# Optimization experiments

Hardware: AMD Instinct MI355X
Metric: run time of the kernel (lower is better)

The kernel has to match this reference:

```python
import jax, jax.numpy as jnp
import numpy as np

NUM_FEATURES = 602
NUM_CLASSES = 41
HIDDEN = 8
HEADS1 = 8
HEADS2 = 1
N_NODES = 100000
N_EDGES = 1600000
NEG_SLOPE = 0.2  # PyG GATConv default leaky_relu slope
EPS = 1e-16      # PyG softmax denominator epsilon


def gat_conv(x, edge_index, W, att_src, att_dst, bias, heads, out_ch, concat):
    """Faithful PyG GATConv forward (eval mode, dropout disabled).
    x: [N, F_in], edge_index: [2, E] with row0=src, row1=dst.
    W: [F_in, heads*out_ch], att_src/att_dst: [heads, out_ch], bias: [heads*out_ch] or [out_ch].
    """
    N = x.shape[0]
    h = (x @ W).reshape(N, heads, out_ch)              # [N, H, C]
    a_src = jnp.einsum('nhc,hc->nh', h, att_src)       # [N, H]
    a_dst = jnp.einsum('nhc,hc->nh', h, att_dst)       # [N, H]
    src, dst = edge_index[0], edge_index[1]
    e = jax.nn.leaky_relu(a_src[src] + a_dst[dst], NEG_SLOPE)  # [E, H]
    # segment softmax over incoming edges of each dst node
    m = jax.ops.segment_max(e, dst, num_segments=N)    # [N, H]
    e = jnp.exp(e - m[dst])
    denom = jax.ops.segment_sum(e, dst, num_segments=N)  # [N, H]
    alpha = e / (denom[dst] + EPS)                     # [E, H]
    msg = h[src] * alpha[:, :, None]                   # [E, H, C]
    out = jax.ops.segment_sum(msg, dst, num_segments=N)  # [N, H, C]
    if concat:
        out = out.reshape(N, heads * out_ch)
    else:
        out = out.mean(axis=1)
    return out + bias


def setup_inputs() -> dict:
    key = jax.random.key(0)
    ks = jax.random.split(key, 10)
    x = jax.random.normal(ks[0], (N_NODES, NUM_FEATURES), dtype=jnp.float32)
    edge_index = jax.random.randint(ks[1], (2, N_EDGES), 0, N_NODES, dtype=jnp.int64)
    s = 0.1
    W1 = jax.random.normal(ks[2], (NUM_FEATURES, HEADS1 * HIDDEN), dtype=jnp.float32) * s
    att_src1 = jax.random.normal(ks[3], (HEADS1, HIDDEN), dtype=jnp.float32) * s
    att_dst1 = jax.random.normal(ks[4], (HEADS1, HIDDEN), dtype=jnp.float32) * s
    b1 = jnp.zeros((HEADS1 * HIDDEN,), dtype=jnp.float32)
    W2 = jax.random.normal(ks[5], (HEADS1 * HIDDEN, HEADS2 * NUM_CLASSES), dtype=jnp.float32) * s
    att_src2 = jax.random.normal(ks[6], (HEADS2, NUM_CLASSES), dtype=jnp.float32) * s
    att_dst2 = jax.random.normal(ks[7], (HEADS2, NUM_CLASSES), dtype=jnp.float32) * s
    b2 = jnp.zeros((NUM_CLASSES,), dtype=jnp.float32)
    return {"x": x, "edge_index": edge_index, "W1": W1, "att_src1": att_src1,
            "att_dst1": att_dst1, "b1": b1, "W2": W2, "att_src2": att_src2,
            "att_dst2": att_dst2, "b2": b2}


def reference(x, edge_index, W1, att_src1, att_dst1, b1, W2, att_src2, att_dst2, b2):
    # eval mode: all F.dropout calls are identity
    h = gat_conv(x, edge_index, W1, att_src1, att_dst1, b1, HEADS1, HIDDEN, concat=True)
    h = jax.nn.elu(h)
    h = gat_conv(h, edge_index, W2, att_src2, att_dst2, b2, HEADS2, NUM_CLASSES, concat=False)
    return jax.nn.log_softmax(h, axis=1)
```

## Files before the change

### kernel.cpp

```cpp
#include <hip/hip_runtime.h>
#include <math.h>

#define NN 100000
#define NE 1600000
#define F_IN 602
#define H1 8
#define C1 8
#define F_MID 64
#define NC 41
#define H2_LD 48
#define NEG_SLOPE 0.2f
#define WT_LD 640
#define GB1 ((NN + 63) / 64)
#define DGB 1024
#define ATB ((NN * H1 + 255) / 256)

#define LRELU(x) fmaxf((x), NEG_SLOPE * (x))

typedef __attribute__((ext_vector_type(8))) short short8;
typedef __attribute__((ext_vector_type(4))) float f32x4;

__device__ inline unsigned short f2bf(float f) {
    unsigned u = __builtin_bit_cast(unsigned, f);
    unsigned r = (u + 0x7FFFu + ((u >> 16) & 1u)) >> 16;
    return (unsigned short)r;
}
__device__ inline float bf2f(unsigned short u) {
    unsigned v = ((unsigned)u) << 16;
    return __builtin_bit_cast(float, v);
}

__global__ void zero_kernel(int4* __restrict__ p, int n4)
{
    int i = blockIdx.x * blockDim.x + threadIdx.x;
    if (i < n4) p[i] = make_int4(0, 0, 0, 0);
}

__global__ void prep_wt_kernel(const float* __restrict__ W, unsigned short* __restrict__ Wt)
{
    int idx = blockIdx.x * blockDim.x + threadIdx.x;
    if (idx >= F_MID * WT_LD) return;
    int col = idx / WT_LD, k = idx % WT_LD;
    Wt[idx] = (k < F_IN) ? f2bf(W[k * F_MID + col]) : (unsigned short)0;
}

__global__ __launch_bounds__(256) void mega1_kernel(
    const float* __restrict__ x, const unsigned short* __restrict__ Wt,
    unsigned short* __restrict__ h1b,
    const int* __restrict__ dst, int* __restrict__ deg, int* __restrict__ rank,
    int N, int E)
{
    __shared__ unsigned short As[64][40];
    __shared__ unsigned short Bs[64][40];

    int bid = blockIdx.x;
    int t = threadIdx.x;

    if (bid < DGB) {
        for (int e = bid * 256 + t; e < E; e += DGB * 256)
            rank[e] = atomicAdd(&deg[dst[e]], 1);
        return;
    }

    int lane = t & 63;
    int w = t >> 6;
    int l16 = lane & 15, lg = lane >> 4;
    int n0 = (bid - DGB) * 64;

    int arow = t >> 2, aseg = t & 3;
    int grow = n0 + arow;
    const float* xrow = x + (size_t)(grow < N ? grow : 0) * F_IN + aseg * 8;
    int bcol = t >> 2;
    const unsigned short* wrow = Wt + (size_t)bcol * WT_LD + aseg * 8;

    f32x4 acc[4] = {};
    float2 av[4];
    uint4  bv;

    #pragma unroll
    for (int i = 0; i < 4; ++i) av[i] = *(const float2*)(xrow + i * 2);
    bv = *(const uint4*)(wrow);

    for (int kt = 0; kt < 19; ++kt) {
        __syncthreads();
        {
            unsigned short tmp[8];
            #pragma unroll
            for (int i = 0; i < 4; ++i) {
                tmp[i * 2]     = f2bf(av[i].x);
                tmp[i * 2 + 1] = f2bf(av[i].y);
            }
            *(uint4*)(&As[arow][aseg * 8]) = *(uint4*)tmp;
            *(uint4*)(&Bs[bcol][aseg * 8]) = bv;
        }
        __syncthreads();

        if (kt < 18) {
            int k0 = (kt + 1) * 32;
            if (kt + 1 < 18) {
                #pragma unroll
                for (int i = 0; i < 4; ++i) av[i] = *(const float2*)(xrow + k0 + i * 2);
            } else {
                #pragma unroll
                for (int i = 0; i < 4; ++i) {
                    int k = k0 + aseg * 8 + i * 2;
                    float a = (k < F_IN)     ? xrow[k0 + i * 2]     : 0.f;
                    float b = (k + 1 < F_IN) ? xrow[k0 + i * 2 + 1] : 0.f;
                    av[i] = make_float2(a, b);
                }
            }
            bv = *(const uint4*)(wrow + k0);
        }

        short8 afrag = *(const short8*)(&As[w * 16 + l16][lg * 8]);
        short8 bfrag[4];
        #pragma unroll
        for (int n = 0; n < 4; ++n)
            bfrag[n] = *(const short8*)(&Bs[n * 16 + l16][lg * 8]);
        #pragma unroll
        for (int n = 0; n < 4; ++n)
            acc[n] = __builtin_amdgcn_mfma_f32_16x16x32_bf16(afrag, bfrag[n], acc[n], 0, 0, 0);
    }

    #pragma unroll
    for (int r = 0; r < 4; ++r) {
        int row = n0 + w * 16 + lg * 4 + r;
        if (row < N) {
            #pragma unroll
            for (int n = 0; n < 4; ++n)
                h1b[(size_t)row * F_MID + n * 16 + l16] = f2bf(acc[n][r]);
        }
    }
}

__global__ void scan1_kernel(const int* __restrict__ deg, int* __restrict__ bsum, int N)
{
    int b = blockIdx.x, t = threadIdx.x;
    int base = b * 1024 + t * 16;
    int s = 0;
    #pragma unroll
    for (int i = 0; i < 16; ++i) { int idx = base + i; if (idx < N) s += deg[idx]; }
    #pragma unroll
    for (int o = 32; o > 0; o >>= 1) s += __shfl_down(s, o);
    if (t == 0) bsum[b] = s;
}

__global__ void scan2_kernel(const int* __restrict__ bsum, int* __restrict__ boff,
                             int nb, int* __restrict__ offs, int N, int E)
{
    __shared__ int buf[128];
    int t = threadIdx.x;
    int v = (t < nb) ? bsum[t] : 0;
    buf[t] = v;
    __syncthreads();
    for (int o = 1; o < 128; o <<= 1) {
        int u = (t >= o) ? buf[t - o] : 0;
        __syncthreads();
        buf[t] += u;
        __syncthreads();
    }
    if (t < nb) boff[t] = buf[t] - v;
    if (t == 0) offs[N] = E;
}

__global__ void scan3_kernel(const int* __restrict__ deg, const int* __restrict__ boff,
                             int* __restrict__ offs, int N)
{
    int b = blockIdx.x, t = threadIdx.x;
    int base = b * 1024 + t * 16;
    int loc[16];
    int s = 0;
    #pragma unroll
    for (int i = 0; i < 16; ++i) {
        int idx = base + i;
        loc[i] = (idx < N) ? deg[idx] : 0;
        s += loc[i];
    }
    int inc = s;
    #pragma unroll
    for (int o = 1; o < 64; o <<= 1) {
        int u = __shfl_up(inc, o);
        if (t >= o) inc += u;
    }
    int run = inc - s + boff[b];
    #pragma unroll
    for (int i = 0; i < 16; ++i) {
        int idx = base + i;
        if (idx < N) offs[idx] = run;
        run += loc[i];
    }
}

__global__ void mega2_kernel(
    const unsigned short* __restrict__ h1b,
    const float* __restrict__ attD,
    float* __restrict__ adst,
    const int* __restrict__ src, const int* __restrict__ dst,
    const int* __restrict__ rank, const int* __restrict__ offs,
    int* __restrict__ srcs, int N, int E)
{
    int bid = blockIdx.x, t = threadIdx.x;
    if (bid < DGB) {
        for (int e = bid * 256 + t; e < E; e += DGB * 256)
            srcs[offs[dst[e]] + rank[e]] = src[e];
        return;
    }
    int idx = (bid - DGB) * 256 + t;
    if (idx >= N * H1) return;
    int n = idx >> 3, hh = idx & 7;
    float d = 0.f;
    #pragma unroll
    for (int c = 0; c < C1; ++c)
        d += bf2f(h1b[n * F_MID + hh * C1 + c]) * attD[hh * C1 + c];
    adst[idx] = d;
}

__global__ void agg1_kernel(const int* __restrict__ offs, const int* __restrict__ srcs,
                            const unsigned short* __restrict__ h1b,
                            const float* __restrict__ attS,
                            const float* __restrict__ adst,
                            const float* __restrict__ b1,
                            float* __restrict__ out1, int N)
{
    int wave = (blockIdx.x * blockDim.x + threadIdx.x) >> 6;
    int lane = threadIdx.x & 63;
    if (wave >= N) return;
    int n = wave;
    int hh = lane >> 3;
    int beg = offs[n], end = offs[n + 1];
    float ad = adst[n * H1 + hh];
    float attv = attS[lane];

    float m = -INFINITY, den = 0.f, acc = 0.f;
    int i = beg;
    for (; i + 8 <= end; i += 8) {
        int s[8];
        #pragma unroll
        for (int j = 0; j < 8; ++j) s[j] = srcs[i + j];
        float v[8];
        #pragma unroll
        for (int j = 0; j < 8; ++j) v[j] = bf2f(h1b[(size_t)s[j] * F_MID + lane]);
        float e[8];
        #pragma unroll
        for (int j = 0; j < 8; ++j) {
            float tt = v[j] * attv;
            tt += __shfl_xor(tt, 1);
            tt += __shfl_xor(tt, 2);
            tt += __shfl_xor(tt, 4);
            e[j] = LRELU(tt + ad);
        }
        float m8 = fmaxf(fmaxf(fmaxf(e[0], e[1]), fmaxf(e[2], e[3])),
                         fmaxf(fmaxf(e[4], e[5]), fmaxf(e[6], e[7])));
        float mn = fmaxf(m, m8);
        float sc = __expf(m - mn);
        float p[8];
        #pragma unroll
        for (int j = 0; j < 8; ++j) p[j] = __expf(e[j] - mn);
        den = den * sc + (((p[0] + p[1]) + (p[2] + p[3])) + ((p[4] + p[5]) + (p[6] + p[7])));
        acc = acc * sc + (((p[0] * v[0] + p[1] * v[1]) + (p[2] * v[2] + p[3] * v[3]))
                        + ((p[4] * v[4] + p[5] * v[5]) + (p[6] * v[6] + p[7] * v[7])));
        m = mn;
    }
    for (; i < end; ++i) {
        int s = srcs[i];
        float hv = bf2f(h1b[(size_t)s * F_MID + lane]);
        float tt = hv * attv;
        tt += __shfl_xor(tt, 1);
        tt += __shfl_xor(tt, 2);
        tt += __shfl_xor(tt, 4);
        float e = LRELU(tt + ad);
        float mn = fmaxf(m, e);
        float sc = __expf(m - mn);
        float p  = __expf(e - mn);
        den = den * sc + p;
        acc = acc * sc + p * hv;
        m = mn;
    }
    float inv = 1.f / (den + 1e-16f);
    float v = acc * inv + b1[lane];
    out1[n * F_MID + lane] = v > 0.f ? v : expm1f(v);
}

__global__ __launch_bounds__(256) void gemm2_kernel(
    const float* __restrict__ out1, const float* __restrict__ W2,
    float* __restrict__ h2p, int N)
{
    __shared__ float ws[F_MID * NC];
    for (int i = threadIdx.x; i < F_MID * NC; i += 256) ws[i] = W2[i];
    __syncthreads();
    int idx = blockIdx.x * blockDim.x + threadIdx.x;
    if (idx >= N * NC) return;
    int n = idx / NC, j = idx % NC;
    const float* row = out1 + n * F_MID;
    float acc = 0.f;
    #pragma unroll
    for (int k = 0; k < F_MID; ++k) acc += row[k] * ws[k * NC + j];
    h2p[(size_t)n * H2_LD + j] = acc;
}

__global__ void attn2_kernel(float* __restrict__ h2p,
                             const float* __restrict__ attS,
                             const float* __restrict__ attD,
                             float* __restrict__ adst, int N)
{
    int n = blockIdx.x * blockDim.x + threadIdx.x;
    if (n >= N) return;
    float s = 0.f, d = 0.f;
    #pragma unroll
    for (int j = 0; j < NC; ++j) {
        float v = h2p[(size_t)n * H2_LD + j];
        s += v * attS[j];
        d += v * attD[j];
    }
    h2p[(size_t)n * H2_LD + NC] = s;
    adst[n] = d;
}

__global__ void agg2_kernel(const int* __restrict__ offs, const int* __restrict__ srcs,
                            const float* __restrict__ h2p,
                            const float* __restrict__ adst,
                            const float* __restrict__ b2,
                            float* __restrict__ out, int N)
{
    int wave = (blockIdx.x * blockDim.x + threadIdx.x) >> 6;
    int lane = threadIdx.x & 63;
    if (wave >= N) return;
    int n = wave;
    int beg = offs[n], end = offs[n + 1];
    float ad = adst[n];
    bool act = lane < NC;
    int li = act ? lane : NC;

    float m = -INFINITY, den = 0.f, acc = 0.f;
    int i = beg;
    for (; i + 8 <= end; i += 8) {
        int s[8];
        #pragma unroll
        for (int j = 0; j < 8; ++j) s[j] = srcs[i + j];
        float hv[8];
        #pragma unroll
        for (int j = 0; j < 8; ++j) hv[j] = h2p[(size_t)s[j] * H2_LD + li];
        float a[8];
        #pragma unroll
        for (int j = 0; j < 8; ++j) a[j] = __shfl(hv[j], NC);
        float e[8];
        #pragma unroll
        for (int j = 0; j < 8; ++j) e[j] = LRELU(a[j] + ad);
        float m8 = fmaxf(fmaxf(fmaxf(e[0], e[1]), fmaxf(e[2], e[3])),
                         fmaxf(fmaxf(e[4], e[5]), fmaxf(e[6], e[7])));
        float mn = fmaxf(m, m8);
        float sc = __expf(m - mn);
        float p[8];
        #pragma unroll
        for (int j = 0; j < 8; ++j) p[j] = __expf(e[j] - mn);
        den = den * sc + (((p[0] + p[1]) + (p[2] + p[3])) + ((p[4] + p[5]) + (p[6] + p[7])));
        acc = acc * sc + (((p[0] * hv[0] + p[1] * hv[1]) + (p[2] * hv[2] + p[3] * hv[3]))
                        + ((p[4] * hv[4] + p[5] * hv[5]) + (p[6] * hv[6] + p[7] * hv[7])));
        m = mn;
    }
    for (; i < end; ++i) {
        int s = srcs[i];
        float hv = h2p[(size_t)s * H2_LD + li];
        float a = __shfl(hv, NC);
        float e = LRELU(a + ad);
        float mn = fmaxf(m, e);
        float sc = __expf(m - mn);
        float p  = __expf(e - mn);
        den = den * sc + p;
        acc = acc * sc + p * hv;
        m = mn;
    }
    float inv = 1.f / (den + 1e-16f);
    float v = act ? acc * inv + b2[lane] : -INFINITY;
    float mm = v;
    #pragma unroll
    for (int o = 32; o > 0; o >>= 1) mm = fmaxf(mm, __shfl_xor(mm, o));
    float ex = act ? __expf(v - mm) : 0.f;
    float S = ex;
    #pragma unroll
    for (int o = 32; o > 0; o >>= 1) S += __shfl_xor(S, o);
    if (act) out[n * NC + lane] = v - mm - logf(S);
}

extern "C" void kernel_launch(void* const* d_in, const int* in_sizes, int n_in,
                              void* d_out, int out_size, void* d_ws, size_t ws_size,
                              hipStream_t stream)
{
    const float* x     = (const float*)d_in[0];
    const int*   ei    = (const int*)  d_in[1];
    const float* W1    = (const float*)d_in[2];
    const float* attS1 = (const float*)d_in[3];
    const float* attD1 = (const float*)d_in[4];
    const float* b1    = (const float*)d_in[5];
    const float* W2    = (const float*)d_in[6];
    const float* attS2 = (const float*)d_in[7];
    const float* attD2 = (const float*)d_in[8];
    const float* b2    = (const float*)d_in[9];
    float* out = (float*)d_out;

    const int N = NN, E = NE;
    const int* src = ei;
    const int* dst = ei + E;

    char* p = (char*)d_ws;
    auto alloc = [&](size_t bytes) { char* r = p; p += (bytes + 255) & ~255ull; return r; };
    unsigned short* h1b = (unsigned short*)alloc((size_t)N * F_MID * 2);
    float* adst1 = (float*)alloc((size_t)N * H1 * 4);
    float* out1  = (float*)alloc((size_t)N * F_MID * 4);
    float* h2p   = (float*)alloc((size_t)N * H2_LD * 4);
    float* adst2 = (float*)alloc((size_t)N * 4);
    int*   deg   = (int*)alloc((size_t)N * 4);
    int*   rank  = (int*)alloc((size_t)E * 4);
    int*   offs  = (int*)alloc((size_t)(N + 1) * 4);
    int*   srcs  = (int*)alloc((size_t)E * 4);
    unsigned short* Wt = (unsigned short*)alloc((size_t)F_MID * WT_LD * 2);
    const int NB = (N + 1023) / 1024;
    int*   bsum  = (int*)alloc((size_t)NB * 4);
    int*   boff  = (int*)alloc((size_t)NB * 4);

    zero_kernel<<<(N / 4 + 255) / 256, 256, 0, stream>>>((int4*)deg, N / 4);
    prep_wt_kernel<<<(F_MID * WT_LD + 255) / 256, 256, 0, stream>>>(W1, Wt);
    mega1_kernel<<<DGB + GB1, 256, 0, stream>>>(x, Wt, h1b, dst, deg, rank, N, E);
    scan1_kernel<<<NB, 64, 0, stream>>>(deg, bsum, N);
    scan2_kernel<<<1, 128, 0, stream>>>(bsum, boff, NB, offs, N, E);
    scan3_kernel<<<NB, 64, 0, stream>>>(deg, boff, offs, N);
    mega2_kernel<<<DGB + ATB, 256, 0, stream>>>(
        h1b, attD1, adst1, src, dst, rank, offs, srcs, N, E);
    agg1_kernel<<<(N * 64 + 255) / 256, 256, 0, stream>>>(
        offs, srcs, h1b, attS1, adst1, b1, out1, N);
    gemm2_kernel<<<(N * NC + 255) / 256, 256, 0, stream>>>(out1, W2, h2p, N);
    attn2_kernel<<<(N + 255) / 256, 256, 0, stream>>>(h2p, attS2, attD2, adst2, N);
    agg2_kernel<<<(N * 64 + 255) / 256, 256, 0, stream>>>(offs, srcs, h2p, adst2, b2, out, N);
}
```

Before: 412.0 us.

## Pipeline GEMM loads via async global_load_lds with triple-buffered LDS slab

The first-layer x@W GEMM now uses `global_load_lds` to copy x (fp32) and Wt (bf16) tiles straight into a three-stage LDS ring. It waits with explicit vmcnt and barriers instead of staging through registers with a double `__syncthreads` per step. The fp32-to-bf16 conversion moves to after the LDS read. The final partial K tile is loaded directly from global memory. This is meant to hide global memory latency and cut register staging, but each x load instruction now touches 64 different rows with 4-byte elements, which may hurt coalescing.

```diff
diff --git a/kernel.cpp b/kernel.cpp
--- a/kernel.cpp
+++ b/kernel.cpp
@@ -16,6 +16,8 @@
 #define ATB ((NN * H1 + 255) / 256)
 
 #define LRELU(x) fmaxf((x), NEG_SLOPE * (x))
+#define GLOBAL_AS __attribute__((address_space(1)))
+#define LDS_AS    __attribute__((address_space(3)))
 
 typedef __attribute__((ext_vector_type(8))) short short8;
 typedef __attribute__((ext_vector_type(4))) float f32x4;
@@ -50,8 +52,7 @@
     const int* __restrict__ dst, int* __restrict__ deg, int* __restrict__ rank,
     int N, int E)
 {
-    __shared__ unsigned short As[64][40];
-    __shared__ unsigned short Bs[64][40];
+    __shared__ __align__(16) unsigned char slab[3 * 12288];
 
     int bid = blockIdx.x;
     int t = threadIdx.x;
@@ -67,56 +68,71 @@
     int l16 = lane & 15, lg = lane >> 4;
     int n0 = (bid - DGB) * 64;
 
-    int arow = t >> 2, aseg = t & 3;
-    int grow = n0 + arow;
-    const float* xrow = x + (size_t)(grow < N ? grow : 0) * F_IN + aseg * 8;
-    int bcol = t >> 2;
-    const unsigned short* wrow = Wt + (size_t)bcol * WT_LD + aseg * 8;
+    int arow = n0 + lane;  if (arow >= N) arow = N - 1;
+    const float* xl = x + (size_t)arow * F_IN;
+    const unsigned short* wl = Wt + (size_t)lane * WT_LD;
+
+    auto issue = [&](int k0, int s) {
+        unsigned char* sb = slab + s * 12288;
+        #pragma unroll
+        for (int i = 0; i < 8; ++i)
+            __builtin_amdgcn_global_load_lds(
+                (const GLOBAL_AS void*)(xl + k0 + w * 8 + i),
+                (LDS_AS void*)(sb + (w * 8 + i) * 256), 4, 0, 0);
+        __builtin_amdgcn_global_load_lds(
+            (const GLOBAL_AS void*)(wl + k0 + w * 8),
+            (LDS_AS void*)(sb + 8192 + w * 1024), 16, 0, 0);
+    };
 
     f32x4 acc[4] = {};
-    float2 av[4];
-    uint4  bv;
-
-    #pragma unroll
-    for (int i = 0; i < 4; ++i) av[i] = *(const float2*)(xrow + i * 2);
-    bv = *(const uint4*)(wrow);
-
-    for (int kt = 0; kt < 19; ++kt) {
-        __syncthreads();
-        {
-            unsigned short tmp[8];
-            #pragma unroll
-            for (int i = 0; i < 4; ++i) {
-                tmp[i * 2]     = f2bf(av[i].x);
-                tmp[i * 2 + 1] = f2bf(av[i].y);
-            }
-            *(uint4*)(&As[arow][aseg * 8]) = *(uint4*)tmp;
-            *(uint4*)(&Bs[bcol][aseg * 8]) = bv;
+
+    issue(0, 0); issue(32, 1); issue(64, 2);
+    asm volatile("s_waitcnt vmcnt(18)" ::: "memory");
+    __builtin_amdgcn_s_barrier();
+
+    for (int kt = 0; kt <= 17; ++kt) {
+        int s = kt % 3;
+        const unsigned char* sb = slab + s * 12288;
+
+        float af[8];
+        #pragma unroll
+        for (int j = 0; j < 8; ++j)
+            af[j] = *(const float*)(sb + (((lg * 8 + j) * 64) + (w * 16 + l16)) * 4);
+        short8 afrag;
+        #pragma unroll
+        for (int j = 0; j < 8; ++j) afrag[j] = (short)f2bf(af[j]);
+        short8 bfrag[4];
+        #pragma unroll
+        for (int n = 0; n < 4; ++n)
+            bfrag[n] = *(const short8*)(sb + 8192 + (lg * 64 + n * 16 + l16) * 16);
+        #pragma unroll
+        for (int n = 0; n < 4; ++n)
+            acc[n] = __builtin_amdgcn_mfma_f32_16x16x32_bf16(afrag, bfrag[n], acc[n], 0, 0, 0);
+
+        __builtin_amdgcn_s_barrier();
+
+        if (kt + 3 <= 17) issue((kt + 3) * 32, s);
+
+        if (kt <= 14)      asm volatile("s_waitcnt vmcnt(18)" ::: "memory");
+        else if (kt == 15) asm volatile("s_waitcnt vmcnt(9)"  ::: "memory");
+        else               asm volatile("s_waitcnt vmcnt(0)"  ::: "memory");
+        __builtin_amdgcn_s_barrier();
+    }
+
+    {
+        const int k0 = 576;
+        int r = n0 + w * 16 + l16;  if (r >= N) r = N - 1;
+        const float* xr = x + (size_t)r * F_IN;
+        short8 afrag;
+        #pragma unroll
+        for (int i = 0; i < 8; ++i) {
+            int k = k0 + lg * 8 + i;
+            afrag[i] = (short)f2bf(k < F_IN ? xr[k] : 0.f);
         }
-        __syncthreads();
-
-        if (kt < 18) {
-            int k0 = (kt + 1) * 32;
-            if (kt + 1 < 18) {
-                #pragma unroll
-                for (int i = 0; i < 4; ++i) av[i] = *(const float2*)(xrow + k0 + i * 2);
-            } else {
-                #pragma unroll
-                for (int i = 0; i < 4; ++i) {
-                    int k = k0 + aseg * 8 + i * 2;
-                    float a = (k < F_IN)     ? xrow[k0 + i * 2]     : 0.f;
-                    float b = (k + 1 < F_IN) ? xrow[k0 + i * 2 + 1] : 0.f;
-                    av[i] = make_float2(a, b);
-                }
-            }
-            bv = *(const uint4*)(wrow + k0);
-        }
-
-        short8 afrag = *(const short8*)(&As[w * 16 + l16][lg * 8]);
         short8 bfrag[4];
         #pragma unroll
         for (int n = 0; n < 4; ++n)
-            bfrag[n] = *(const short8*)(&Bs[n * 16 + l16][lg * 8]);
+            bfrag[n] = *(const short8*)(Wt + (size_t)(n * 16 + l16) * WT_LD + k0 + lg * 8);
         #pragma unroll
         for (int n = 0; n < 4; ++n)
             acc[n] = __builtin_amdgcn_mfma_f32_16x16x32_bf16(afrag, bfrag[n], acc[n], 0, 0, 0);
```

Measured after the change: 484.9 us. 1.18x slower.

## Double GEMM K-tile to 64 and merge zeroing into weight-prep kernel

Applied to the files above, without the earlier changes.

The first-layer GEMM now stages 64 K-elements per iteration instead of 32, so it needs 10 loop iterations instead of 19 and half as many barrier pairs. Each iteration issues two MFMA k-steps, and each thread loads twice as much data per stage. The degree-zeroing kernel is folded into the weight transpose kernel, removing one launch. The larger tiles add register and LDS use, which may lower occupancy.

```diff
diff --git a/kernel.cpp b/kernel.cpp
--- a/kernel.cpp
+++ b/kernel.cpp
@@ -30,18 +30,17 @@
     return __builtin_bit_cast(float, v);
 }
 
-__global__ void zero_kernel(int4* __restrict__ p, int n4)
-{
-    int i = blockIdx.x * blockDim.x + threadIdx.x;
-    if (i < n4) p[i] = make_int4(0, 0, 0, 0);
-}
-
-__global__ void prep_wt_kernel(const float* __restrict__ W, unsigned short* __restrict__ Wt)
+__global__ void prep_kernel(const float* __restrict__ W, unsigned short* __restrict__ Wt,
+                            int4* __restrict__ degv, int ndeg4)
 {
     int idx = blockIdx.x * blockDim.x + threadIdx.x;
-    if (idx >= F_MID * WT_LD) return;
-    int col = idx / WT_LD, k = idx % WT_LD;
-    Wt[idx] = (k < F_IN) ? f2bf(W[k * F_MID + col]) : (unsigned short)0;
+    if (idx < F_MID * WT_LD) {
+        int col = idx / WT_LD, k = idx % WT_LD;
+        Wt[idx] = (k < F_IN) ? f2bf(W[k * F_MID + col]) : (unsigned short)0;
+    } else {
+        int z = idx - F_MID * WT_LD;
+        if (z < ndeg4) degv[z] = make_int4(0, 0, 0, 0);
+    }
 }
 
 __global__ __launch_bounds__(256) void mega1_kernel(
@@ -50,8 +49,8 @@
     const int* __restrict__ dst, int* __restrict__ deg, int* __restrict__ rank,
     int N, int E)
 {
-    __shared__ unsigned short As[64][40];
-    __shared__ unsigned short Bs[64][40];
+    __shared__ unsigned short As[64][72];
+    __shared__ unsigned short Bs[64][72];
 
     int bid = blockIdx.x;
     int t = threadIdx.x;
@@ -69,57 +68,64 @@
 
     int arow = t >> 2, aseg = t & 3;
     int grow = n0 + arow;
-    const float* xrow = x + (size_t)(grow < N ? grow : 0) * F_IN + aseg * 8;
+    const float* xrow = x + (size_t)(grow < N ? grow : 0) * F_IN + aseg * 16;
     int bcol = t >> 2;
-    const unsigned short* wrow = Wt + (size_t)bcol * WT_LD + aseg * 8;
+    const unsigned short* wrow = Wt + (size_t)bcol * WT_LD + aseg * 16;
 
     f32x4 acc[4] = {};
-    float2 av[4];
-    uint4  bv;
-
-    #pragma unroll
-    for (int i = 0; i < 4; ++i) av[i] = *(const float2*)(xrow + i * 2);
-    bv = *(const uint4*)(wrow);
-
-    for (int kt = 0; kt < 19; ++kt) {
+    float2 av[8];
+    uint4  bv[2];
+
+    #pragma unroll
+    for (int i = 0; i < 8; ++i) av[i] = *(const float2*)(xrow + i * 2);
+    bv[0] = *(const uint4*)(wrow);
+    bv[1] = *(const uint4*)(wrow + 8);
+
+    for (int kt = 0; kt < 10; ++kt) {
         __syncthreads();
         {
-            unsigned short tmp[8];
+            unsigned short tmp[16];
             #pragma unroll
-            for (int i = 0; i < 4; ++i) {
+            for (int i = 0; i < 8; ++i) {
                 tmp[i * 2]     = f2bf(av[i].x);
                 tmp[i * 2 + 1] = f2bf(av[i].y);
             }
-            *(uint4*)(&As[arow][aseg * 8]) = *(uint4*)tmp;
-            *(uint4*)(&Bs[bcol][aseg * 8]) = bv;
+            *(uint4*)(&As[arow][aseg * 16])     = ((const uint4*)tmp)[0];
+            *(uint4*)(&As[arow][aseg * 16 + 8]) = ((const uint4*)tmp)[1];
+            *(uint4*)(&Bs[bcol][aseg * 16])     = bv[0];
+            *(uint4*)(&Bs[bcol][aseg * 16 + 8]) = bv[1];
         }
         __syncthreads();
 
-        if (kt < 18) {
-            int k0 = (kt + 1) * 32;
-            if (kt + 1 < 18) {
+        if (kt < 9) {
+            int k0 = (kt + 1) * 64;
+            if (kt + 1 < 9) {
                 #pragma unroll
-                for (int i = 0; i < 4; ++i) av[i] = *(const float2*)(xrow + k0 + i * 2);
+                for (int i = 0; i < 8; ++i) av[i] = *(const float2*)(xrow + k0 + i * 2);
             } else {
                 #pragma unroll
-                for (int i = 0; i < 4; ++i) {
-                    int k = k0 + aseg * 8 + i * 2;
+                for (int i = 0; i < 8; ++i) {
+                    int k = k0 + aseg * 16 + i * 2;
                     float a = (k < F_IN)     ? xrow[k0 + i * 2]     : 0.f;
                     float b = (k + 1 < F_IN) ? xrow[k0 + i * 2 + 1] : 0.f;
                     av[i] = make_float2(a, b);
                 }
             }
-            bv = *(const uint4*)(wrow + k0);
+            bv[0] = *(const uint4*)(wrow + k0);
+            bv[1] = *(const uint4*)(wrow + k0 + 8);
         }
 
-        short8 afrag = *(const short8*)(&As[w * 16 + l16][lg * 8]);
-        short8 bfrag[4];
-        #pragma unroll
-        for (int n = 0; n < 4; ++n)
-            bfrag[n] = *(const short8*)(&Bs[n * 16 + l16][lg * 8]);
-        #pragma unroll
-        for (int n = 0; n < 4; ++n)
-            acc[n] = __builtin_amdgcn_mfma_f32_16x16x32_bf16(afrag, bfrag[n], acc[n], 0, 0, 0);
+        #pragma unroll
+        for (int ks = 0; ks < 2; ++ks) {
+            short8 afrag = *(const short8*)(&As[w * 16 + l16][ks * 32 + lg * 8]);
+            short8 bfrag[4];
+            #pragma unroll
+            for (int n = 0; n < 4; ++n)
+                bfrag[n] = *(const short8*)(&Bs[n * 16 + l16][ks * 32 + lg * 8]);
+            #pragma unroll
+            for (int n = 0; n < 4; ++n)
+                acc[n] = __builtin_amdgcn_mfma_f32_16x16x32_bf16(afrag, bfrag[n], acc[n], 0, 0, 0);
+        }
     }
 
     #pragma unroll
@@ -418,8 +424,9 @@
     int*   bsum  = (int*)alloc((size_t)NB * 4);
     int*   boff  = (int*)alloc((size_t)NB * 4);
 
-    zero_kernel<<<(N / 4 + 255) / 256, 256, 0, stream>>>((int4*)deg, N / 4);
-    prep_wt_kernel<<<(F_MID * WT_LD + 255) / 256, 256, 0, stream>>>(W1, Wt);
+    const int ndeg4 = N / 4;
+    prep_kernel<<<(F_MID * WT_LD + ndeg4 + 255) / 256, 256, 0, stream>>>(
+        W1, Wt, (int4*)deg, ndeg4);
     mega1_kernel<<<DGB + GB1, 256, 0, stream>>>(x, Wt, h1b, dst, deg, rank, N, E);
     scan1_kernel<<<NB, 64, 0, stream>>>(deg, bsum, N);
     scan2_kernel<<<1, 128, 0, stream>>>(bsum, boff, NB, offs, N, E);
```

New measurement: 460.1 us. +11.7%, slower.
